# Optimization experiments

Hardware: AMD Instinct MI355X
Metric: run time of the kernel (lower is better)

The kernel has to match this reference:

```python
import jax, jax.numpy as jnp
import numpy as np

B = 16384
OUT = 128          # output_size (per conditioning frame)
NCOND = 3
HID = 32           # MLP3 hidden
LSTM_H = 64        # lstm_output_size (input == hidden)
NPRED = 25
EPS = 1e-5


def setup_inputs() -> dict:
    key = jax.random.key(0)
    ks = jax.random.split(key, 20)
    d = {
        "x0": jax.random.normal(ks[0], (B, OUT), jnp.float32),
        "x1": jax.random.normal(ks[1], (B, OUT), jnp.float32),
        "x2": jax.random.normal(ks[2], (B, OUT), jnp.float32),
        # MLP3: Linear(384->32), BN, ReLU, Linear(32->32), BN, ReLU, Linear(32->64)
        "W1": jax.random.normal(ks[3], (HID, OUT * NCOND), jnp.float32) * 0.05,
        "b1": jnp.full((HID,), 0.03, jnp.float32),
        "g1": jnp.ones((HID,), jnp.float32),
        "beta1": jnp.zeros((HID,), jnp.float32),
        "W2": jax.random.normal(ks[4], (HID, HID), jnp.float32) * 0.1,
        "b2": jnp.full((HID,), 0.03, jnp.float32),
        "g2": jnp.ones((HID,), jnp.float32),
        "beta2": jnp.zeros((HID,), jnp.float32),
        "W3": jax.random.normal(ks[5], (LSTM_H, HID), jnp.float32) * 0.1,
        "b3": jnp.full((LSTM_H,), 0.03, jnp.float32),
        # LSTM (torch gate order i,f,g,o): weight_ih (4H,H), weight_hh (4H,H)
        "Wih": jax.random.normal(ks[6], (4 * LSTM_H, LSTM_H), jnp.float32) * 0.08,
        "Whh": jax.random.normal(ks[7], (4 * LSTM_H, LSTM_H), jnp.float32) * 0.08,
        "bih": jnp.zeros((4 * LSTM_H,), jnp.float32),
        "bhh": jnp.zeros((4 * LSTM_H,), jnp.float32),
    }
    return d


def _bn_train(h, g, b):
    # BatchNorm1d in training mode: biased batch statistics
    m = jnp.mean(h, axis=0)
    v = jnp.var(h, axis=0)
    return g * (h - m) * jax.lax.rsqrt(v + EPS) + b


def _lstm_step(inp, h, c, Wih, Whh, bih, bhh):
    gates = inp @ Wih.T + bih + h @ Whh.T + bhh  # (B, 4H)
    i, f, g, o = jnp.split(gates, 4, axis=1)
    c_new = jax.nn.sigmoid(f) * c + jax.nn.sigmoid(i) * jnp.tanh(g)
    h_new = jax.nn.sigmoid(o) * jnp.tanh(c_new)
    return h_new, c_new


def reference(x0, x1, x2, W1, b1, g1, beta1, W2, b2, g2, beta2, W3, b3,
              Wih, Whh, bih, bhh):
    x = jnp.concatenate([x0, x1, x2], axis=1)          # (B, 384)
    h = jax.nn.relu(_bn_train(x @ W1.T + b1, g1, beta1))
    h = jax.nn.relu(_bn_train(h @ W2.T + b2, g2, beta2))
    m = h @ W3.T + b3                                   # (B, 64)

    h0 = jnp.zeros((m.shape[0], LSTM_H), m.dtype)
    c0 = jnp.zeros_like(h0)
    # initial conditioning step (output discarded except as state/next input)
    h1, c1 = _lstm_step(m, h0, c0, Wih, Whh, bih, bhh)

    def step(carry, _):
        hh, cc = carry
        # loop feeds previous output back as input; output == h for 1-layer LSTM
        hn, cn = _lstm_step(hh, hh, cc, Wih, Whh, bih, bhh)
        return (hn, cn), hn

    _, outs = jax.lax.scan(step, (h1, c1), None, length=NPRED)  # (25, B, 64)
    return jnp.transpose(outs, (1, 0, 2))                        # (B, 25, 64)
```

## Files before the change

### kernel.cpp

```cpp
#include <hip/hip_runtime.h>


#define EPSV 1e-5f
#define LOG2E 1.4426950408889634f
#define K2    2.8853900817779268f

typedef __attribute__((ext_vector_type(8))) short bf16x8;
typedef __attribute__((ext_vector_type(4))) float f32x4;

__device__ __forceinline__ float rcp_f(float x) { return __builtin_amdgcn_rcpf(x); }
__device__ __forceinline__ void split_bf16(float x, ushort& hi, ushort& lo) {
    unsigned xb = __builtin_bit_cast(unsigned, x);
    hi = (ushort)(xb >> 16);
    float hif = __builtin_bit_cast(float, xb & 0xffff0000u);
    unsigned lb = __builtin_bit_cast(unsigned, x - hif);
    lo = (ushort)(lb >> 16);
}

__global__ __launch_bounds__(256) void k_prep(
    const float* __restrict__ Wih, const float* __restrict__ Whh,
    const float* __restrict__ bih, const float* __restrict__ bhh,
    const float* __restrict__ W1, const float* __restrict__ W2,
    ushort* __restrict__ Wih_hi, ushort* __restrict__ Wih_lo,
    ushort* __restrict__ Wsum_hi, ushort* __restrict__ Wsum_lo,
    ushort* __restrict__ W1hi, ushort* __restrict__ W1lo,
    ushort* __restrict__ W2hi, ushort* __restrict__ W2lo,
    float* __restrict__ bsum)
{
    int i = blockIdx.x * 256 + threadIdx.x;
    ushort h, l;
    if (i < 16384) {
        int j = i >> 6;
        float sc = (j >= 128 && j < 192) ? K2 : LOG2E;
        float wi  = Wih[i] * sc;
        float wsv = (Wih[i] + Whh[i]) * sc;
        split_bf16(wi, h, l);  Wih_hi[i] = h;  Wih_lo[i] = l;
        split_bf16(wsv, h, l); Wsum_hi[i] = h; Wsum_lo[i] = l;
    }
    if (i < 12288) { split_bf16(W1[i], h, l); W1hi[i] = h; W1lo[i] = l; }
    if (i < 1024)  { split_bf16(W2[i], h, l); W2hi[i] = h; W2lo[i] = l; }
    if (i < 256) {
        float sc = (i >= 128 && i < 192) ? K2 : LOG2E;
        bsum[i] = (bih[i] + bhh[i]) * sc;
    }
}

__global__ __launch_bounds__(256) void k_red(const float* __restrict__ part,
                                             const float* __restrict__ g,
                                             const float* __restrict__ be,
                                             float* __restrict__ scsh) {
    __shared__ float rs[8][32], rq[8][32];
    const int t = threadIdx.x, ch = t & 31, sl = t >> 5;
    float s = 0.f, q = 0.f;
    #pragma unroll 4
    for (int i = 0; i < 128; ++i) {
        int b = sl * 128 + i;
        s += part[b * 32 + ch];
        q += part[32768 + b * 32 + ch];
    }
    rs[sl][ch] = s; rq[sl][ch] = q;
    __syncthreads();
    if (t < 32) {
        float ss = 0.f, qq = 0.f;
        #pragma unroll
        for (int k = 0; k < 8; ++k) { ss += rs[k][t]; qq += rq[k][t]; }
        float mu = ss * (1.f / 16384.f);
        float va = qq * (1.f / 16384.f) - mu * mu;
        float sc = g[t] * rsqrtf(va + EPSV);
        scsh[t] = sc; scsh[32 + t] = be[t] - mu * sc;
    }
}

__global__ __launch_bounds__(256) void k_mlp1(
    const float* __restrict__ x0, const float* __restrict__ x1, const float* __restrict__ x2,
    const ushort* __restrict__ W1hi, const ushort* __restrict__ W1lo,
    const float* __restrict__ b1,
    float* __restrict__ pre, float* __restrict__ st1p)
{
    __shared__ __align__(16) ushort xhi[32 * 392];
    __shared__ __align__(16) ushort xlo[32 * 392];
    const int tid = threadIdx.x;
    const int r0  = blockIdx.x * 32;

    for (int a = 0; a < 3; ++a) {
        const float* xp = (a == 0) ? x0 : (a == 1) ? x1 : x2;
        const float4* src = (const float4*)(xp + (size_t)r0 * 128);
        #pragma unroll
        for (int it = 0; it < 4; ++it) {
            int i = it * 256 + tid;
            int row = i >> 5, c4 = i & 31;
            float4 v = src[i];
            ushort h0, l0, h1, l1, h2, l2, h3, l3;
            split_bf16(v.x, h0, l0); split_bf16(v.y, h1, l1);
            split_bf16(v.z, h2, l2); split_bf16(v.w, h3, l3);
            int ofs = row * 392 + a * 128 + c4 * 4;
            *(ushort4*)&xhi[ofs] = make_ushort4(h0, h1, h2, h3);
            *(ushort4*)&xlo[ofs] = make_ushort4(l0, l1, l2, l3);
        }
    }
    __syncthreads();

    const int lane = tid & 63, l15 = lane & 15, lg = lane >> 4, q = tid >> 6;
    const int m0 = (q & 1) * 16, n0 = (q >> 1) * 16;
    const float bias = b1[n0 + l15];
    f32x4 acc = {bias, bias, bias, bias};
    #pragma unroll
    for (int kt = 0; kt < 12; ++kt) {
        bf16x8 ahi = *(const bf16x8*)&xhi[(m0 + l15) * 392 + kt * 32 + lg * 8];
        bf16x8 alo = *(const bf16x8*)&xlo[(m0 + l15) * 392 + kt * 32 + lg * 8];
        bf16x8 bhi = *(const bf16x8*)(W1hi + (size_t)(n0 + l15) * 384 + kt * 32 + lg * 8);
        bf16x8 blo = *(const bf16x8*)(W1lo + (size_t)(n0 + l15) * 384 + kt * 32 + lg * 8);
        acc = __builtin_amdgcn_mfma_f32_16x16x32_bf16(ahi, bhi, acc, 0, 0, 0);
        acc = __builtin_amdgcn_mfma_f32_16x16x32_bf16(ahi, blo, acc, 0, 0, 0);
        acc = __builtin_amdgcn_mfma_f32_16x16x32_bf16(alo, bhi, acc, 0, 0, 0);
    }
    #pragma unroll
    for (int rg = 0; rg < 4; ++rg)
        pre[(size_t)(r0 + m0 + lg * 4 + rg) * 32 + n0 + l15] = acc[rg];
    float s  = (acc[0] + acc[1]) + (acc[2] + acc[3]);
    float sq = (acc[0] * acc[0] + acc[1] * acc[1]) + (acc[2] * acc[2] + acc[3] * acc[3]);
    s  += __shfl_xor(s, 16);  s  += __shfl_xor(s, 32);
    sq += __shfl_xor(sq, 16); sq += __shfl_xor(sq, 32);
    if (lg == 0) {
        int slot = (blockIdx.x * 2 + (q & 1)) * 32 + n0 + l15;
        st1p[slot] = s;
        st1p[32768 + slot] = sq;
    }
}

__global__ __launch_bounds__(256) void k_mlp2(
    float* __restrict__ pre, const float* __restrict__ scsh1,
    const ushort* __restrict__ W2hi, const ushort* __restrict__ W2lo,
    const float* __restrict__ b2, float* __restrict__ st2p)
{
    __shared__ __align__(16) ushort hhi[32 * 40];
    __shared__ __align__(16) ushort hlo[32 * 40];
    __shared__ float bnsc[32], bnsh[32];
    const int tid = threadIdx.x;
    const int r0  = blockIdx.x * 32;

    if (tid < 32) { bnsc[tid] = scsh1[tid]; bnsh[tid] = scsh1[32 + tid]; }
    __syncthreads();
    {
        int row = tid >> 3, c4 = tid & 7;
        float4 v = ((const float4*)(pre + (size_t)r0 * 32))[tid];
        float e0 = fmaxf(fmaf(v.x, bnsc[c4 * 4 + 0], bnsh[c4 * 4 + 0]), 0.f);
        float e1 = fmaxf(fmaf(v.y, bnsc[c4 * 4 + 1], bnsh[c4 * 4 + 1]), 0.f);
        float e2 = fmaxf(fmaf(v.z, bnsc[c4 * 4 + 2], bnsh[c4 * 4 + 2]), 0.f);
        float e3 = fmaxf(fmaf(v.w, bnsc[c4 * 4 + 3], bnsh[c4 * 4 + 3]), 0.f);
        ushort h0, l0, h1, l1, h2, l2, h3, l3;
        split_bf16(e0, h0, l0); split_bf16(e1, h1, l1);
        split_bf16(e2, h2, l2); split_bf16(e3, h3, l3);
        int ofs = row * 40 + c4 * 4;
        *(ushort4*)&hhi[ofs] = make_ushort4(h0, h1, h2, h3);
        *(ushort4*)&hlo[ofs] = make_ushort4(l0, l1, l2, l3);
    }
    __syncthreads();

    const int lane = tid & 63, l15 = lane & 15, lg = lane >> 4, q = tid >> 6;
    const int m0 = (q & 1) * 16, n0 = (q >> 1) * 16;
    const float bias = b2[n0 + l15];
    f32x4 acc = {bias, bias, bias, bias};
    bf16x8 ahi = *(const bf16x8*)&hhi[(m0 + l15) * 40 + lg * 8];
    bf16x8 alo = *(const bf16x8*)&hlo[(m0 + l15) * 40 + lg * 8];
    bf16x8 bhi = *(const bf16x8*)(W2hi + (size_t)(n0 + l15) * 32 + lg * 8);
    bf16x8 blo = *(const bf16x8*)(W2lo + (size_t)(n0 + l15) * 32 + lg * 8);
    acc = __builtin_amdgcn_mfma_f32_16x16x32_bf16(ahi, bhi, acc, 0, 0, 0);
    acc = __builtin_amdgcn_mfma_f32_16x16x32_bf16(ahi, blo, acc, 0, 0, 0);
    acc = __builtin_amdgcn_mfma_f32_16x16x32_bf16(alo, bhi, acc, 0, 0, 0);

    #pragma unroll
    for (int rg = 0; rg < 4; ++rg)
        pre[(size_t)(r0 + m0 + lg * 4 + rg) * 32 + n0 + l15] = acc[rg];
    float s  = (acc[0] + acc[1]) + (acc[2] + acc[3]);
    float sq = (acc[0] * acc[0] + acc[1] * acc[1]) + (acc[2] * acc[2] + acc[3] * acc[3]);
    s  += __shfl_xor(s, 16);  s  += __shfl_xor(s, 32);
    sq += __shfl_xor(sq, 16); sq += __shfl_xor(sq, 32);
    if (lg == 0) {
        int slot = (blockIdx.x * 2 + (q & 1)) * 32 + n0 + l15;
        st2p[slot] = s;
        st2p[32768 + slot] = sq;
    }
}

__global__ __launch_bounds__(256, 2) void k_lstm(
    const float* __restrict__ pre, const float* __restrict__ scsh2,
    const float* __restrict__ W3, const float* __restrict__ b3,
    const ushort* __restrict__ Wih_hi, const ushort* __restrict__ Wih_lo,
    const ushort* __restrict__ Wsum_hi, const ushort* __restrict__ Wsum_lo,
    const float* __restrict__ bsum, float* __restrict__ out)
{
    __shared__ __align__(16) ushort hhi[2][2][16][72];
    __shared__ __align__(16) ushort hlo[2][2][16][72];
    __shared__ float bn2sc[32], bn2sh[32];
    const int tid  = threadIdx.x;
    const int lane = tid & 63, l15 = lane & 15, lg = lane >> 4, q = tid >> 6;
    const int r0   = blockIdx.x * 32;

    if (tid < 32) { bn2sc[tid] = scsh2[tid]; bn2sh[tid] = scsh2[32 + tid]; }
    __syncthreads();

    {
        const int row = tid & 31, seg = tid >> 5;
        float h2[32];
        const float4* pr = (const float4*)(pre + (size_t)(r0 + row) * 32);
        #pragma unroll
        for (int j4 = 0; j4 < 8; ++j4) {
            float4 v = pr[j4];
            h2[j4 * 4 + 0] = v.x; h2[j4 * 4 + 1] = v.y;
            h2[j4 * 4 + 2] = v.z; h2[j4 * 4 + 3] = v.w;
        }
        #pragma unroll
        for (int j = 0; j < 32; ++j) h2[j] = fmaxf(fmaf(h2[j], bn2sc[j], bn2sh[j]), 0.f);
        #pragma unroll
        for (int uu = 0; uu < 8; ++uu) {
            int u = seg * 8 + uu;
            const float* w = W3 + u * 32;
            float a0 = 0.f, a1 = 0.f, a2 = 0.f, a3 = 0.f;
            #pragma unroll
            for (int k = 0; k < 32; k += 4) {
                a0 = fmaf(h2[k + 0], w[k + 0], a0);
                a1 = fmaf(h2[k + 1], w[k + 1], a1);
                a2 = fmaf(h2[k + 2], w[k + 2], a2);
                a3 = fmaf(h2[k + 3], w[k + 3], a3);
            }
            float m = b3[u] + ((a0 + a1) + (a2 + a3));
            ushort mh, ml; split_bf16(m, mh, ml);
            hhi[row >> 4][0][row & 15][u] = mh;
            hlo[row >> 4][0][row & 15][u] = ml;
        }
    }

    float bias[4];
    #pragma unroll
    for (int nt = 0; nt < 4; ++nt) bias[nt] = bsum[nt * 64 + q * 16 + l15];
    float cA[4] = {0.f, 0.f, 0.f, 0.f}, cB[4] = {0.f, 0.f, 0.f, 0.f};

    bf16x8 Bhi[4][2], Blo[4][2];
    const size_t wofs = (size_t)(q * 16 + l15) * 64 + lg * 8;
    #pragma unroll
    for (int nt = 0; nt < 4; ++nt)
        #pragma unroll
        for (int kt = 0; kt < 2; ++kt) {
            Bhi[nt][kt] = *(const bf16x8*)(Wih_hi + (size_t)nt * 4096 + wofs + kt * 32);
            Blo[nt][kt] = *(const bf16x8*)(Wih_lo + (size_t)nt * 4096 + wofs + kt * 32);
        }
    __syncthreads();

#define MFMA_GATES(ACC, G, BUF)                                                  \
    {                                                                            \
        _Pragma("unroll")                                                        \
        for (int nt = 0; nt < 4; ++nt)                                           \
            ACC[nt] = (f32x4){bias[nt], bias[nt], bias[nt], bias[nt]};           \
        _Pragma("unroll")                                                        \
        for (int kt = 0; kt < 2; ++kt) {                                         \
            bf16x8 ahi = *(const bf16x8*)&hhi[G][BUF][l15][kt * 32 + lg * 8];    \
            bf16x8 alo = *(const bf16x8*)&hlo[G][BUF][l15][kt * 32 + lg * 8];    \
            _Pragma("unroll")                                                    \
            for (int nt = 0; nt < 4; ++nt) {                                     \
                ACC[nt] = __builtin_amdgcn_mfma_f32_16x16x32_bf16(ahi, Bhi[nt][kt], ACC[nt], 0, 0, 0); \
                ACC[nt] = __builtin_amdgcn_mfma_f32_16x16x32_bf16(ahi, Blo[nt][kt], ACC[nt], 0, 0, 0); \
                ACC[nt] = __builtin_amdgcn_mfma_f32_16x16x32_bf16(alo, Bhi[nt][kt], ACC[nt], 0, 0, 0); \
            }                                                                    \
        }                                                                        \
    }

#define ACT(ACC, C, G, WBUF, SLOT, WRLDS)                                        \
    {                                                                            \
        const int u = q * 16 + l15;                                              \
        _Pragma("unroll")                                                        \
        for (int rg = 0; rg < 4; ++rg) {                                         \
            int row = lg * 4 + rg;                                               \
            float iv = ACC[0][rg], fv = ACC[1][rg];                              \
            float gv = ACC[2][rg], ov = ACC[3][rg];                              \
            float Af = __builtin_amdgcn_exp2f(-fv);                              \
            float Ai = __builtin_amdgcn_exp2f(-iv);                              \
            float Bg = __builtin_amdgcn_exp2f(gv);                               \
            float sig = (Bg - 1.f) * rcp_f((1.f + Ai) * (Bg + 1.f));             \
            float cc = C[rg] * rcp_f(1.f + Af) + sig;                            \
            C[rg] = cc;                                                          \
            float Ao = __builtin_amdgcn_exp2f(-ov);                              \
            float C2 = __builtin_amdgcn_exp2f(cc * K2);                          \
            float hn = (C2 - 1.f) * rcp_f((1.f + Ao) * (C2 + 1.f));              \
            if (WRLDS) {                                                         \
                ushort hh, hl; split_bf16(hn, hh, hl);                           \
                hhi[G][WBUF][row][u] = hh;                                       \
                hlo[G][WBUF][row][u] = hl;                                       \
            }                                                                    \
            if ((SLOT) >= 0)                                                     \
                out[(size_t)(r0 + (G)*16 + row) * 1600 + (size_t)(SLOT) * 64 + u] = hn; \
        }                                                                        \
    }

    f32x4 accA[4], accB[4];

    MFMA_GATES(accA, 0, 0);
    MFMA_GATES(accB, 1, 0);
    #pragma unroll
    for (int nt = 0; nt < 4; ++nt)
        #pragma unroll
        for (int kt = 0; kt < 2; ++kt) {
            Bhi[nt][kt] = *(const bf16x8*)(Wsum_hi + (size_t)nt * 4096 + wofs + kt * 32);
            Blo[nt][kt] = *(const bf16x8*)(Wsum_lo + (size_t)nt * 4096 + wofs + kt * 32);
        }
    ACT(accA, cA, 0, 1, -1, 1);
    __syncthreads();

    #pragma unroll 1
    for (int s = 1; s <= 25; ++s) {
        const int rb = s & 1, wb = rb ^ 1;
        MFMA_GATES(accA, 0, rb);
        ACT(accB, cB, 1, rb, s - 2, 1);
        __syncthreads();
        MFMA_GATES(accB, 1, rb);
        ACT(accA, cA, 0, wb, s - 1, 1);
        __syncthreads();
    }
    ACT(accB, cB, 1, 0, 24, 0);

#undef MFMA_GATES
#undef ACT
}

extern "C" void kernel_launch(void* const* d_in, const int* in_sizes, int n_in,
                              void* d_out, int out_size, void* d_ws, size_t ws_size,
                              hipStream_t stream) {
    const float* x0   = (const float*)d_in[0];
    const float* x1   = (const float*)d_in[1];
    const float* x2   = (const float*)d_in[2];
    const float* W1   = (const float*)d_in[3];
    const float* b1   = (const float*)d_in[4];
    const float* g1   = (const float*)d_in[5];
    const float* be1  = (const float*)d_in[6];
    const float* W2   = (const float*)d_in[7];
    const float* b2   = (const float*)d_in[8];
    const float* g2   = (const float*)d_in[9];
    const float* be2  = (const float*)d_in[10];
    const float* W3   = (const float*)d_in[11];
    const float* b3   = (const float*)d_in[12];
    const float* Wih  = (const float*)d_in[13];
    const float* Whh  = (const float*)d_in[14];
    const float* bih  = (const float*)d_in[15];
    const float* bhh  = (const float*)d_in[16];

    float* ws    = (float*)d_ws;
    float* pre   = ws;
    float* st1p  = ws + 524288;
    float* st2p  = ws + 589824;
    float* scsh1 = ws + 655360;
    float* scsh2 = ws + 655424;
    float* bsum  = ws + 655488;
    ushort* ub   = (ushort*)(ws + 655744);
    ushort* Wih_hi  = ub;
    ushort* Wih_lo  = ub + 16384;
    ushort* Wsum_hi = ub + 32768;
    ushort* Wsum_lo = ub + 49152;
    ushort* W1hi    = ub + 65536;
    ushort* W1lo    = ub + 77824;
    ushort* W2hi    = ub + 90112;
    ushort* W2lo    = ub + 91136;

    hipLaunchKernelGGL(k_prep, dim3(64), dim3(256), 0, stream,
                       Wih, Whh, bih, bhh, W1, W2,
                       Wih_hi, Wih_lo, Wsum_hi, Wsum_lo, W1hi, W1lo, W2hi, W2lo, bsum);
    hipLaunchKernelGGL(k_mlp1, dim3(512), dim3(256), 0, stream,
                       x0, x1, x2, W1hi, W1lo, b1, pre, st1p);
    hipLaunchKernelGGL(k_red, dim3(1), dim3(256), 0, stream, st1p, g1, be1, scsh1);
    hipLaunchKernelGGL(k_mlp2, dim3(512), dim3(256), 0, stream,
                       pre, scsh1, W2hi, W2lo, b2, st2p);
    hipLaunchKernelGGL(k_red, dim3(1), dim3(256), 0, stream, st2p, g2, be2, scsh2);
    hipLaunchKernelGGL(k_lstm, dim3(512), dim3(256), 0, stream,
                       pre, scsh2, W3, b3,
                       Wih_hi, Wih_lo, Wsum_hi, Wsum_lo, bsum, (float*)d_out);
}
```

Measured before the change: 100.9 us.

## Parallelize BN stat reduction across channel blocks and precompute LSTM output pointers

The batch-norm statistics reduction goes from a single block to 32 blocks, one per channel. Each thread sums four partials, then a shared-memory tree reduction finishes the sum, which shortens the serial chain in the tiny reduction kernels. The LSTM kernel also precomputes per-row output base pointers, so the address math for each output store becomes a constant offset. The cost is strided, uncoalesced reads of the partials in the reduction and more live registers in the LSTM kernel.

```diff
diff --git a/kernel.cpp b/kernel.cpp
--- a/kernel.cpp
+++ b/kernel.cpp
@@ -49,25 +49,24 @@
                                              const float* __restrict__ g,
                                              const float* __restrict__ be,
                                              float* __restrict__ scsh) {
-    __shared__ float rs[8][32], rq[8][32];
-    const int t = threadIdx.x, ch = t & 31, sl = t >> 5;
-    float s = 0.f, q = 0.f;
-    #pragma unroll 4
-    for (int i = 0; i < 128; ++i) {
-        int b = sl * 128 + i;
-        s += part[b * 32 + ch];
-        q += part[32768 + b * 32 + ch];
-    }
-    rs[sl][ch] = s; rq[sl][ch] = q;
-    __syncthreads();
-    if (t < 32) {
-        float ss = 0.f, qq = 0.f;
-        #pragma unroll
-        for (int k = 0; k < 8; ++k) { ss += rs[k][t]; qq += rq[k][t]; }
-        float mu = ss * (1.f / 16384.f);
-        float va = qq * (1.f / 16384.f) - mu * mu;
-        float sc = g[t] * rsqrtf(va + EPSV);
-        scsh[t] = sc; scsh[32 + t] = be[t] - mu * sc;
+    __shared__ float rs[256], rq[256];
+    const int ch = blockIdx.x, t = threadIdx.x;
+    float s = (part[t * 32 + ch] + part[(t + 256) * 32 + ch]) +
+              (part[(t + 512) * 32 + ch] + part[(t + 768) * 32 + ch]);
+    float q = (part[32768 + t * 32 + ch] + part[32768 + (t + 256) * 32 + ch]) +
+              (part[32768 + (t + 512) * 32 + ch] + part[32768 + (t + 768) * 32 + ch]);
+    rs[t] = s; rq[t] = q;
+    __syncthreads();
+    #pragma unroll
+    for (int off = 128; off > 0; off >>= 1) {
+        if (t < off) { rs[t] += rs[t + off]; rq[t] += rq[t + off]; }
+        __syncthreads();
+    }
+    if (t == 0) {
+        float mu = rs[0] * (1.f / 16384.f);
+        float va = rq[0] * (1.f / 16384.f) - mu * mu;
+        float sc = g[ch] * rsqrtf(va + EPSV);
+        scsh[ch] = sc; scsh[32 + ch] = be[ch] - mu * sc;
     }
 }
 
@@ -235,6 +234,14 @@
     #pragma unroll
     for (int nt = 0; nt < 4; ++nt) bias[nt] = bsum[nt * 64 + q * 16 + l15];
     float cA[4] = {0.f, 0.f, 0.f, 0.f}, cB[4] = {0.f, 0.f, 0.f, 0.f};
+
+    float* obA[4];
+    float* obB[4];
+    #pragma unroll
+    for (int rg = 0; rg < 4; ++rg) {
+        obA[rg] = out + (size_t)(r0 + lg * 4 + rg) * 1600 + (q * 16 + l15);
+        obB[rg] = out + (size_t)(r0 + 16 + lg * 4 + rg) * 1600 + (q * 16 + l15);
+    }
 
     bf16x8 Bhi[4][2], Blo[4][2];
     const size_t wofs = (size_t)(q * 16 + l15) * 64 + lg * 8;
@@ -265,7 +272,7 @@
         }                                                                        \
     }
 
-#define ACT(ACC, C, G, WBUF, SLOT, WRLDS)                                        \
+#define ACT(ACC, C, G, WBUF, OB, SLOT, WRLDS)                                    \
     {                                                                            \
         const int u = q * 16 + l15;                                              \
         _Pragma("unroll")                                                        \
@@ -288,7 +295,7 @@
                 hlo[G][WBUF][row][u] = hl;                                       \
             }                                                                    \
             if ((SLOT) >= 0)                                                     \
-                out[(size_t)(r0 + (G)*16 + row) * 1600 + (size_t)(SLOT) * 64 + u] = hn; \
+                OB[rg][(size_t)(SLOT) * 64] = hn;                                \
         }                                                                        \
     }
 
@@ -303,20 +310,20 @@
             Bhi[nt][kt] = *(const bf16x8*)(Wsum_hi + (size_t)nt * 4096 + wofs + kt * 32);
             Blo[nt][kt] = *(const bf16x8*)(Wsum_lo + (size_t)nt * 4096 + wofs + kt * 32);
         }
-    ACT(accA, cA, 0, 1, -1, 1);
+    ACT(accA, cA, 0, 1, obA, -1, 1);
     __syncthreads();
 
     #pragma unroll 1
     for (int s = 1; s <= 25; ++s) {
         const int rb = s & 1, wb = rb ^ 1;
         MFMA_GATES(accA, 0, rb);
-        ACT(accB, cB, 1, rb, s - 2, 1);
+        ACT(accB, cB, 1, rb, obB, s - 2, 1);
         __syncthreads();
         MFMA_GATES(accB, 1, rb);
-        ACT(accA, cA, 0, wb, s - 1, 1);
+        ACT(accA, cA, 0, wb, obA, s - 1, 1);
         __syncthreads();
     }
-    ACT(accB, cB, 1, 0, 24, 0);
+    ACT(accB, cB, 1, 0, obB, 24, 0);
 
 #undef MFMA_GATES
 #undef ACT
@@ -365,10 +372,10 @@
                        Wih_hi, Wih_lo, Wsum_hi, Wsum_lo, W1hi, W1lo, W2hi, W2lo, bsum);
     hipLaunchKernelGGL(k_mlp1, dim3(512), dim3(256), 0, stream,
                        x0, x1, x2, W1hi, W1lo, b1, pre, st1p);
-    hipLaunchKernelGGL(k_red, dim3(1), dim3(256), 0, stream, st1p, g1, be1, scsh1);
+    hipLaunchKernelGGL(k_red, dim3(32), dim3(256), 0, stream, st1p, g1, be1, scsh1);
     hipLaunchKernelGGL(k_mlp2, dim3(512), dim3(256), 0, stream,
                        pre, scsh1, W2hi, W2lo, b2, st2p);
-    hipLaunchKernelGGL(k_red, dim3(1), dim3(256), 0, stream, st2p, g2, be2, scsh2);
+    hipLaunchKernelGGL(k_red, dim3(32), dim3(256), 0, stream, st2p, g2, be2, scsh2);
     hipLaunchKernelGGL(k_lstm, dim3(512), dim3(256), 0, stream,
                        pre, scsh2, W3, b3,
                        Wih_hi, Wih_lo, Wsum_hi, Wsum_lo, bsum, (float*)d_out);
```

Result: faster. 87.81 us (-13.0%).
